# Kernel tuning notes

Measured on AMD Instinct MI355X. Metric: run time of the kernel, lower is better.

## Reference

```python
import jax, jax.numpy as jnp
import numpy as np

B, H, W, D, U = 32, 64, 64, 256, 512


def setup_inputs() -> dict:
    key = jax.random.key(0)
    k1, k2, k3, k4, k5 = jax.random.split(key, 5)
    he_in = np.sqrt(2.0 / D)
    he_u = np.sqrt(2.0 / U)
    return {
        "x": jax.random.normal(k1, (B, H, W, D), dtype=jnp.float32),
        "wax": jax.random.normal(k2, (D, U), dtype=jnp.float32) * he_in,
        "w0": jax.random.normal(k3, (U, U), dtype=jnp.float32) * he_u,
        "w1": jax.random.normal(k4, (U, U), dtype=jnp.float32) * he_u,
        "ba": jax.random.normal(k5, (1, U), dtype=jnp.float32) * 0.01,
    }


def reference(x, wax, w0, w1, ba):
    """2D MDRNN, direction (+1,+1), zero initial state, tanh activation.

    h[i,j] = tanh(x[i,j] @ wax + h[i-1,j] @ w0 + h[i,j-1] @ w1 + ba)
    (out-of-bound neighbors contribute zero, matching the original with
    zero initial state). Returns h at final position (H-1, W-1): (B, U).
    """
    b, h, w, d = x.shape
    u = wax.shape[1]
    # Precompute input contribution for the whole grid: (H, W, B, U)
    zx = jnp.einsum("bhwd,du->hwbu", x, wax) + ba

    def row_step(prev_row, zx_row):
        # prev_row: (W, B, U) = h[i-1, :]; zx_row: (W, B, U)
        pre = zx_row + jnp.einsum("wbu,uv->wbv", prev_row, w0)

        def col_step(h_left, pre_j):
            h_ij = jnp.tanh(pre_j + h_left @ w1)
            return h_ij, h_ij

        _, row = jax.lax.scan(col_step, jnp.zeros((b, u), x.dtype), pre)
        return row, None

    last_row, _ = jax.lax.scan(row_step, jnp.zeros((w, b, u), x.dtype), zx)
    return last_row[-1]  # (B, U)
```

## Files before the change

kernel.cpp:

```cpp
#include <hip/hip_runtime.h>
#include <stdint.h>

#define H_ 64
#define W_ 64
#define D_ 256
#define U_ 512
#define KREC 1024
#define CELL_ELT (32 * U_)

typedef __attribute__((ext_vector_type(8))) _Float16 half8;
typedef __attribute__((ext_vector_type(8))) unsigned short ushort8;
typedef __attribute__((ext_vector_type(4))) float f32x4;

__device__ __forceinline__ unsigned short f2h(float f) {
    _Float16 h = (_Float16)f;
    return __builtin_bit_cast(unsigned short, h);
}

__device__ __forceinline__ int swzo(int r, int o) {
    return o ^ (((r ^ (o >> 7)) & 7) << 4);
}

__global__ void prep_w(const float* __restrict__ w0,
                       const float* __restrict__ w1,
                       unsigned short* __restrict__ wcT2) {
    int n = blockIdx.x;
    for (int k = threadIdx.x; k < KREC; k += blockDim.x) {
        float v = (k < U_) ? w0[(size_t)k * U_ + n] : w1[(size_t)(k - U_) * U_ + n];
        wcT2[(size_t)n * KREC + k] = f2h(v);
    }
}

__global__ void prep_waxT(const float* __restrict__ wax,
                          unsigned short* __restrict__ waxT) {
    int n = blockIdx.x;
    for (int k = threadIdx.x; k < D_; k += blockDim.x)
        waxT[(size_t)n * D_ + k] = f2h(wax[(size_t)k * U_ + n]);
}

__global__ __launch_bounds__(256) void prep_z(
    const float* __restrict__ x,
    const unsigned short* __restrict__ waxT,
    const float* __restrict__ ba,
    unsigned short* __restrict__ zfh)
{
    __shared__ char xs[32 * 512];
    const int cell = blockIdx.x;
    const int t = threadIdx.x, lane = t & 63, wv = t >> 6;
    const int l15 = lane & 15, lh = lane >> 4;
    const int r = t >> 3, c8 = t & 7;

    {
        const float4* src = reinterpret_cast<const float4*>(
            x + (size_t)r * (H_ * W_ * D_) + (size_t)cell * D_ + c8 * 32);
        float4 f[8];
        #pragma unroll
        for (int q = 0; q < 8; ++q) f[q] = src[q];
        #pragma unroll
        for (int s = 0; s < 4; ++s) {
            float4 a = f[2 * s], b = f[2 * s + 1];
            ushort8 o;
            o[0] = f2h(a.x); o[1] = f2h(a.y); o[2] = f2h(a.z); o[3] = f2h(a.w);
            o[4] = f2h(b.x); o[5] = f2h(b.y); o[6] = f2h(b.z); o[7] = f2h(b.w);
            int ob = c8 * 64 + s * 16;
            *reinterpret_cast<ushort8*>(xs + r * 512 + swzo(r, ob)) = o;
        }
    }
    __syncthreads();

    f32x4 zero = {0.f, 0.f, 0.f, 0.f};
    f32x4 acc[2][8];
    #pragma unroll
    for (int m = 0; m < 2; ++m)
        #pragma unroll
        for (int n = 0; n < 8; ++n) acc[m][n] = zero;

    const char* ar0 = xs + l15 * 512;
    const char* ar1 = xs + (16 + l15) * 512;
    #pragma unroll
    for (int ks = 0; ks < 8; ++ks) {
        int ob = ks * 64 + lh * 16;
        int oo = swzo(l15, ob);
        half8 af0 = *reinterpret_cast<const half8*>(ar0 + oo);
        half8 af1 = *reinterpret_cast<const half8*>(ar1 + oo);
        #pragma unroll
        for (int ntg = 0; ntg < 8; ++ntg) {
            int col = wv * 128 + ntg * 16 + l15;
            half8 bf = *reinterpret_cast<const half8*>(waxT + (size_t)col * D_ + ks * 32 + lh * 8);
            acc[0][ntg] = __builtin_amdgcn_mfma_f32_16x16x32_f16(af0, bf, acc[0][ntg], 0, 0, 0);
            acc[1][ntg] = __builtin_amdgcn_mfma_f32_16x16x32_f16(af1, bf, acc[1][ntg], 0, 0, 0);
        }
    }

    #pragma unroll
    for (int s = 0; s < 4; ++s) {
        unsigned short* dst = zfh + (((size_t)cell * 16 + wv * 4 + s) * 64 + lane) * 16;
        float bav0 = ba[wv * 128 + s * 32 + l15];
        float bav1 = ba[wv * 128 + s * 32 + 16 + l15];
        ushort8 oa, ob;
        #pragma unroll
        for (int rr = 0; rr < 4; ++rr) {
            oa[rr]     = f2h(acc[0][s * 2 + 0][rr] + bav0);
            oa[4 + rr] = f2h(acc[0][s * 2 + 1][rr] + bav1);
            ob[rr]     = f2h(acc[1][s * 2 + 0][rr] + bav0);
            ob[4 + rr] = f2h(acc[1][s * 2 + 1][rr] + bav1);
        }
        *reinterpret_cast<ushort8*>(dst)     = oa;
        *reinterpret_cast<ushort8*>(dst + 8) = ob;
    }
}

__global__ __launch_bounds__(256, 1) void mdrnn_persistent(
    const unsigned short* __restrict__ wcT2,
    const unsigned short* __restrict__ zfh,
    unsigned short* __restrict__ hgrid,
    int* flags2,
    float* __restrict__ out)
{
    __shared__ char smb[32 * 2048];
    __shared__ unsigned long long heps64[32 * 32];
    unsigned short* heps16 = reinterpret_cast<unsigned short*>(heps64);

    const int j  = (int)blockIdx.x & 63;
    const int nc = (int)blockIdx.x >> 6;
    const int t = threadIdx.x, lane = t & 63, wv = t >> 6;
    const int l15 = lane & 15, lh = lane >> 4;
    const int r = t >> 3, c8 = t & 7;
    const int gw = nc * 4 + wv;
    const unsigned long long RDY2 = 0x0000000100000001ULL;

    half8 breg[2][32];
    {
        const unsigned short* wb = wcT2 + (size_t)(nc * 128 + wv * 32 + l15) * KREC + lh * 8;
        #pragma unroll
        for (int nt = 0; nt < 2; ++nt)
            #pragma unroll
            for (int ks = 0; ks < 32; ++ks)
                breg[nt][ks] = *reinterpret_cast<const half8*>(wb + (size_t)nt * 16 * KREC + ks * 32);
    }

    #pragma clang loop unroll(disable)
    for (int i = 0; i < H_; ++i) {
        const int cell = i * W_ + j;

        const ushort8* zp = reinterpret_cast<const ushort8*>(
            zfh + (((size_t)cell * 16 + gw) * 64 + lane) * 16);
        ushort8 zv0 = zp[0], zv1 = zp[1];

        if (i > 0 || j > 0) {
            const unsigned long long* fu = reinterpret_cast<const unsigned long long*>(
                flags2 + (size_t)(cell - W_) * 16);
            const unsigned long long* fl = reinterpret_cast<const unsigned long long*>(
                flags2 + (size_t)(cell - 1) * 16);
            const bool nu = (i > 0), nl = (j > 0);
            for (;;) {
                bool ok = true;
                if (nu) {
                    unsigned long long a = __hip_atomic_load(fu,     __ATOMIC_RELAXED, __HIP_MEMORY_SCOPE_AGENT);
                    unsigned long long b = __hip_atomic_load(fu + 1, __ATOMIC_RELAXED, __HIP_MEMORY_SCOPE_AGENT);
                    ok = ok && (a == RDY2) && (b == RDY2);
                }
                if (nl) {
                    unsigned long long a = __hip_atomic_load(fl,     __ATOMIC_RELAXED, __HIP_MEMORY_SCOPE_AGENT);
                    unsigned long long b = __hip_atomic_load(fl + 1, __ATOMIC_RELAXED, __HIP_MEMORY_SCOPE_AGENT);
                    ok = ok && (a == RDY2) && (b == RDY2);
                }
                if (ok) break;
                __builtin_amdgcn_s_sleep(1);
            }
        }
        asm volatile("" ::: "memory");

        if (i > 0) {
            const ushort8* us = reinterpret_cast<const ushort8*>(
                hgrid + (size_t)(cell - W_) * CELL_ELT + (size_t)r * U_ + c8 * 64);
            ushort8 ub[8];
            #pragma unroll
            for (int s = 0; s < 8; ++s) ub[s] = us[s];
            #pragma unroll
            for (int s = 0; s < 8; ++s) {
                int ob = c8 * 128 + s * 16;
                *reinterpret_cast<ushort8*>(smb + r * 2048 + swzo(r, ob)) = ub[s];
            }
        }
        if (j > 0) {
            const ushort8* ls = reinterpret_cast<const ushort8*>(
                hgrid + (size_t)(cell - 1) * CELL_ELT + (size_t)r * U_ + c8 * 64);
            ushort8 lb[8];
            #pragma unroll
            for (int s = 0; s < 8; ++s) lb[s] = ls[s];
            #pragma unroll
            for (int s = 0; s < 8; ++s) {
                int ob = 1024 + c8 * 128 + s * 16;
                *reinterpret_cast<ushort8*>(smb + r * 2048 + swzo(r, ob)) = lb[s];
            }
        }
        __syncthreads();

        f32x4 zero = {0.f, 0.f, 0.f, 0.f};
        f32x4 acc00 = zero, acc01 = zero, acc10 = zero, acc11 = zero;
        const char* ar0 = smb + l15 * 2048;
        const char* ar1 = smb + (16 + l15) * 2048;

#define MSTEP(ks)                                                                                \
        {                                                                                        \
            int ob = (ks) * 64 + lh * 16;                                                        \
            int oo = swzo(l15, ob);                                                              \
            half8 af0 = *reinterpret_cast<const half8*>(ar0 + oo);                               \
            half8 af1 = *reinterpret_cast<const half8*>(ar1 + oo);                               \
            acc00 = __builtin_amdgcn_mfma_f32_16x16x32_f16(af0, breg[0][(ks)], acc00, 0, 0, 0);  \
            acc01 = __builtin_amdgcn_mfma_f32_16x16x32_f16(af0, breg[1][(ks)], acc01, 0, 0, 0);  \
            acc10 = __builtin_amdgcn_mfma_f32_16x16x32_f16(af1, breg[0][(ks)], acc10, 0, 0, 0);  \
            acc11 = __builtin_amdgcn_mfma_f32_16x16x32_f16(af1, breg[1][(ks)], acc11, 0, 0, 0);  \
        }
        if (i > 0) {
            #pragma unroll
            for (int ks = 0; ks < 16; ++ks) MSTEP(ks)
        }
        if (j > 0) {
            #pragma unroll
            for (int ks = 16; ks < 32; ++ks) MSTEP(ks)
        }
#undef MSTEP

        const bool lastcell = (i == H_ - 1) && (j == W_ - 1);
        const int col0 = nc * 128 + wv * 32 + l15;
        const half8 hz0 = __builtin_bit_cast(half8, zv0);
        const half8 hz1 = __builtin_bit_cast(half8, zv1);
        #pragma unroll
        for (int mt = 0; mt < 2; ++mt) {
            f32x4 a0 = mt ? acc10 : acc00;
            f32x4 a1 = mt ? acc11 : acc01;
            half8 hz = mt ? hz1 : hz0;
            #pragma unroll
            for (int rr = 0; rr < 4; ++rr) {
                int row = mt * 16 + lh * 4 + rr;
                float v0 = fminf(fmaxf(a0[rr] + (float)hz[rr],     -15.f), 15.f);
                float v1 = fminf(fmaxf(a1[rr] + (float)hz[4 + rr], -15.f), 15.f);
                float e0 = __expf(2.f * v0), e1 = __expf(2.f * v1);
                float th0 = (e0 - 1.f) / (e0 + 1.f);
                float th1 = (e1 - 1.f) / (e1 + 1.f);
                heps16[row * 128 + wv * 32 + l15]      = f2h(th0);
                heps16[row * 128 + wv * 32 + 16 + l15] = f2h(th1);
                if (lastcell) {
                    out[(size_t)row * U_ + col0]      = th0;
                    out[(size_t)row * U_ + col0 + 16] = th1;
                }
            }
        }
        __syncthreads();

        {
            const int erow = t >> 3, e = t & 7;
            unsigned long long* gq = reinterpret_cast<unsigned long long*>(
                hgrid + (size_t)cell * CELL_ELT + (size_t)erow * U_ + nc * 128);
            #pragma unroll
            for (int q = 0; q < 4; ++q) {
                unsigned long long v = heps64[erow * 32 + q * 8 + e];
                __hip_atomic_store(gq + q * 8 + e, v, __ATOMIC_RELAXED, __HIP_MEMORY_SCOPE_AGENT);
            }
        }

        asm volatile("s_waitcnt vmcnt(0)" ::: "memory");
        __syncthreads();
        if (t == 0)
            __hip_atomic_store(&flags2[(size_t)cell * 16 + nc], 1,
                               __ATOMIC_RELAXED, __HIP_MEMORY_SCOPE_AGENT);
    }
}

extern "C" void kernel_launch(void* const* d_in, const int* in_sizes, int n_in,
                              void* d_out, int out_size, void* d_ws, size_t ws_size,
                              hipStream_t stream) {
    const float* x   = (const float*)d_in[0];
    const float* wax = (const float*)d_in[1];
    const float* w0  = (const float*)d_in[2];
    const float* w1  = (const float*)d_in[3];
    const float* ba  = (const float*)d_in[4];
    float* out = (float*)d_out;

    char* w = (char*)d_ws;
    unsigned short* wcT2   = (unsigned short*)(w);
    unsigned short* waxT   = (unsigned short*)(w + (1u << 20));
    int*            flags2 = (int*)(w + (1u << 20) + (256u << 10));
    unsigned short* zfh    = (unsigned short*)(w + (2u << 20));
    unsigned short* hgrid  = (unsigned short*)(w + (2u << 20) + ((size_t)128 << 20));

    (void)hipMemsetAsync(flags2, 0, (size_t)H_ * W_ * 16 * sizeof(int), stream);
    prep_w   <<<dim3(U_), dim3(256), 0, stream>>>(w0, w1, wcT2);
    prep_waxT<<<dim3(U_), dim3(256), 0, stream>>>(wax, waxT);
    prep_z   <<<dim3(H_ * W_), dim3(256), 0, stream>>>(x, waxT, ba, zfh);
    mdrnn_persistent<<<dim3(W_ * 4), dim3(256), 0, stream>>>(wcT2, zfh, hgrid, flags2, out);
}
```

Before: 996.0 us.

## Group adjacent columns per XCD and poll XCD-local L2 flags for neighbours

```diff
diff --git a/kernel.cpp b/kernel.cpp
--- a/kernel.cpp
+++ b/kernel.cpp
@@ -19,6 +19,18 @@
 
 __device__ __forceinline__ int swzo(int r, int o) {
     return o ^ (((r ^ (o >> 7)) & 7) << 4);
+}
+
+__device__ __forceinline__ int bid_of(int jc, int c) {
+    return (jc >> 3) + ((jc & 7) << 3) + (c << 6);
+}
+
+__device__ __forceinline__ void l2_load2(const unsigned long long* p,
+                                         unsigned long long& a, unsigned long long& b) {
+    asm volatile("global_load_dwordx2 %0, %2, off sc0\n\t"
+                 "global_load_dwordx2 %1, %3, off sc0\n\t"
+                 "s_waitcnt vmcnt(0)"
+                 : "=v"(a), "=v"(b) : "v"(p), "v"(p + 1) : "memory");
 }
 
 __global__ void prep_w(const float* __restrict__ w0,
@@ -79,8 +91,7 @@
     const char* ar1 = xs + (16 + l15) * 512;
     #pragma unroll
     for (int ks = 0; ks < 8; ++ks) {
-        int ob = ks * 64 + lh * 16;
-        int oo = swzo(l15, ob);
+        int oo = swzo(l15, ks * 64 + lh * 16);
         half8 af0 = *reinterpret_cast<const half8*>(ar0 + oo);
         half8 af1 = *reinterpret_cast<const half8*>(ar1 + oo);
         #pragma unroll
@@ -114,21 +125,48 @@
     const unsigned short* __restrict__ wcT2,
     const unsigned short* __restrict__ zfh,
     unsigned short* __restrict__ hgrid,
-    int* flags2,
+    int* flagsLLC, int* flagsL2, int* xcdmap, int* startctr,
     float* __restrict__ out)
 {
     __shared__ char smb[32 * 2048];
     __shared__ unsigned long long heps64[32 * 32];
+    __shared__ int sflag[2];
     unsigned short* heps16 = reinterpret_cast<unsigned short*>(heps64);
 
-    const int j  = (int)blockIdx.x & 63;
-    const int nc = (int)blockIdx.x >> 6;
+    const int blk = (int)blockIdx.x;
+    const int j  = ((blk & 7) << 3) | ((blk >> 3) & 7);
+    const int nc = blk >> 6;
     const int t = threadIdx.x, lane = t & 63, wv = t >> 6;
     const int l15 = lane & 15, lh = lane >> 4;
     const int r = t >> 3, c8 = t & 7;
     const int gw = nc * 4 + wv;
     const unsigned long long RDY2 = 0x0000000100000001ULL;
 
+    __builtin_amdgcn_fence(__ATOMIC_ACQUIRE, "agent");
+    int myxcd;
+    asm volatile("s_getreg_b32 %0, hwreg(HW_REG_XCC_ID)" : "=s"(myxcd));
+    myxcd &= 15;
+    if (t == 0) {
+        __hip_atomic_store(&xcdmap[blk], myxcd + 1, __ATOMIC_RELAXED, __HIP_MEMORY_SCOPE_AGENT);
+        __hip_atomic_fetch_add(startctr, 1, __ATOMIC_RELAXED, __HIP_MEMORY_SCOPE_AGENT);
+        while (__hip_atomic_load(startctr, __ATOMIC_RELAXED, __HIP_MEMORY_SCOPE_AGENT) < 256)
+            __builtin_amdgcn_s_sleep(2);
+        int uf = 1, lf = (j > 0) ? 1 : 0;
+        for (int c = 0; c < 4; ++c) {
+            int v = __hip_atomic_load(&xcdmap[bid_of(j, c)], __ATOMIC_RELAXED, __HIP_MEMORY_SCOPE_AGENT);
+            uf &= (v == myxcd + 1);
+        }
+        if (j > 0)
+            for (int c = 0; c < 4; ++c) {
+                int v = __hip_atomic_load(&xcdmap[bid_of(j - 1, c)], __ATOMIC_RELAXED, __HIP_MEMORY_SCOPE_AGENT);
+                lf &= (v == myxcd + 1);
+            }
+        sflag[0] = uf; sflag[1] = lf;
+    }
+    __syncthreads();
+    const bool uFast = sflag[0] != 0;
+    const bool lFast = sflag[1] != 0;
+
     half8 breg[2][32];
     {
         const unsigned short* wb = wcT2 + (size_t)(nc * 128 + wv * 32 + l15) * KREC + lh * 8;
@@ -148,25 +186,39 @@
         ushort8 zv0 = zp[0], zv1 = zp[1];
 
         if (i > 0 || j > 0) {
-            const unsigned long long* fu = reinterpret_cast<const unsigned long long*>(
-                flags2 + (size_t)(cell - W_) * 16);
-            const unsigned long long* fl = reinterpret_cast<const unsigned long long*>(
-                flags2 + (size_t)(cell - 1) * 16);
             const bool nu = (i > 0), nl = (j > 0);
-            for (;;) {
-                bool ok = true;
-                if (nu) {
-                    unsigned long long a = __hip_atomic_load(fu,     __ATOMIC_RELAXED, __HIP_MEMORY_SCOPE_AGENT);
-                    unsigned long long b = __hip_atomic_load(fu + 1, __ATOMIC_RELAXED, __HIP_MEMORY_SCOPE_AGENT);
-                    ok = ok && (a == RDY2) && (b == RDY2);
+            const unsigned long long* fuF = reinterpret_cast<const unsigned long long*>(
+                flagsL2 + (size_t)(cell - W_) * 16);
+            const unsigned long long* flF = reinterpret_cast<const unsigned long long*>(
+                flagsL2 + (size_t)(cell - 1) * 16);
+            const unsigned long long* fuS = reinterpret_cast<const unsigned long long*>(
+                flagsLLC + (size_t)(cell - W_) * 16);
+            const unsigned long long* flS = reinterpret_cast<const unsigned long long*>(
+                flagsLLC + (size_t)(cell - 1) * 16);
+            bool uok = !nu, lok = !nl;
+            int it = 0;
+            while (!(uok && lok)) {
+                const bool ins = ((it & 63) == 63);
+                if (!uok) {
+                    unsigned long long a, b2;
+                    if (uFast && !ins) l2_load2(fuF, a, b2);
+                    else {
+                        a  = __hip_atomic_load(fuS,     __ATOMIC_RELAXED, __HIP_MEMORY_SCOPE_AGENT);
+                        b2 = __hip_atomic_load(fuS + 1, __ATOMIC_RELAXED, __HIP_MEMORY_SCOPE_AGENT);
+                    }
+                    uok = (a == RDY2) && (b2 == RDY2);
                 }
-                if (nl) {
-                    unsigned long long a = __hip_atomic_load(fl,     __ATOMIC_RELAXED, __HIP_MEMORY_SCOPE_AGENT);
-                    unsigned long long b = __hip_atomic_load(fl + 1, __ATOMIC_RELAXED, __HIP_MEMORY_SCOPE_AGENT);
-                    ok = ok && (a == RDY2) && (b == RDY2);
+                if (!lok) {
+                    unsigned long long a, b2;
+                    if (lFast && !ins) l2_load2(flF, a, b2);
+                    else {
+                        a  = __hip_atomic_load(flS,     __ATOMIC_RELAXED, __HIP_MEMORY_SCOPE_AGENT);
+                        b2 = __hip_atomic_load(flS + 1, __ATOMIC_RELAXED, __HIP_MEMORY_SCOPE_AGENT);
+                    }
+                    lok = (a == RDY2) && (b2 == RDY2);
                 }
-                if (ok) break;
-                __builtin_amdgcn_s_sleep(1);
+                if (!(uok && lok)) __builtin_amdgcn_s_sleep(1);
+                ++it;
             }
         }
         asm volatile("" ::: "memory");
@@ -204,8 +256,7 @@
 
 #define MSTEP(ks)                                                                                \
         {                                                                                        \
-            int ob = (ks) * 64 + lh * 16;                                                        \
-            int oo = swzo(l15, ob);                                                              \
+            int oo = swzo(l15, (ks) * 64 + lh * 16);                                             \
             half8 af0 = *reinterpret_cast<const half8*>(ar0 + oo);                               \
             half8 af1 = *reinterpret_cast<const half8*>(ar1 + oo);                               \
             acc00 = __builtin_amdgcn_mfma_f32_16x16x32_f16(af0, breg[0][(ks)], acc00, 0, 0, 0);  \
@@ -250,21 +301,28 @@
         }
         __syncthreads();
 
-        {
-            const int erow = t >> 3, e = t & 7;
-            unsigned long long* gq = reinterpret_cast<unsigned long long*>(
-                hgrid + (size_t)cell * CELL_ELT + (size_t)erow * U_ + nc * 128);
-            #pragma unroll
-            for (int q = 0; q < 4; ++q) {
-                unsigned long long v = heps64[erow * 32 + q * 8 + e];
-                __hip_atomic_store(gq + q * 8 + e, v, __ATOMIC_RELAXED, __HIP_MEMORY_SCOPE_AGENT);
-            }
-        }
-
+        const int erow = t >> 3, e = t & 7;
+        unsigned long long* gq = reinterpret_cast<unsigned long long*>(
+            hgrid + (size_t)cell * CELL_ELT + (size_t)erow * U_ + nc * 128);
+
+        #pragma unroll
+        for (int q = 0; q < 4; ++q)
+            __hip_atomic_store(gq + q * 8 + e, heps64[erow * 32 + q * 8 + e],
+                               __ATOMIC_RELAXED, __HIP_MEMORY_SCOPE_WORKGROUP);
         asm volatile("s_waitcnt vmcnt(0)" ::: "memory");
         __syncthreads();
         if (t == 0)
-            __hip_atomic_store(&flags2[(size_t)cell * 16 + nc], 1,
+            __hip_atomic_store(&flagsL2[(size_t)cell * 16 + nc], 1,
+                               __ATOMIC_RELAXED, __HIP_MEMORY_SCOPE_WORKGROUP);
+
+        #pragma unroll
+        for (int q = 0; q < 4; ++q)
+            __hip_atomic_store(gq + q * 8 + e, heps64[erow * 32 + q * 8 + e],
+                               __ATOMIC_RELAXED, __HIP_MEMORY_SCOPE_AGENT);
+        asm volatile("s_waitcnt vmcnt(0)" ::: "memory");
+        __syncthreads();
+        if (t == 0)
+            __hip_atomic_store(&flagsLLC[(size_t)cell * 16 + nc], 1,
                                __ATOMIC_RELAXED, __HIP_MEMORY_SCOPE_AGENT);
     }
 }
@@ -280,15 +338,19 @@
     float* out = (float*)d_out;
 
     char* w = (char*)d_ws;
-    unsigned short* wcT2   = (unsigned short*)(w);
-    unsigned short* waxT   = (unsigned short*)(w + (1u << 20));
-    int*            flags2 = (int*)(w + (1u << 20) + (256u << 10));
-    unsigned short* zfh    = (unsigned short*)(w + (2u << 20));
-    unsigned short* hgrid  = (unsigned short*)(w + (2u << 20) + ((size_t)128 << 20));
-
-    (void)hipMemsetAsync(flags2, 0, (size_t)H_ * W_ * 16 * sizeof(int), stream);
+    unsigned short* wcT2     = (unsigned short*)(w);
+    unsigned short* waxT     = (unsigned short*)(w + (1u << 20));
+    int*            flagsLLC = (int*)(w + (1u << 20) + (256u << 10));
+    int*            flagsL2  = (int*)(w + (1u << 20) + (512u << 10));
+    int*            xcdmap   = (int*)(w + (1u << 20) + (768u << 10));
+    int*            startctr = (int*)(w + (1u << 20) + (768u << 10) + 4096);
+    unsigned short* zfh      = (unsigned short*)(w + (2u << 20));
+    unsigned short* hgrid    = (unsigned short*)(w + (2u << 20) + ((size_t)128 << 20));
+
+    (void)hipMemsetAsync(flagsLLC, 0, (768u << 10), stream);
     prep_w   <<<dim3(U_), dim3(256), 0, stream>>>(w0, w1, wcT2);
     prep_waxT<<<dim3(U_), dim3(256), 0, stream>>>(wax, waxT);
     prep_z   <<<dim3(H_ * W_), dim3(256), 0, stream>>>(x, waxT, ba, zfh);
-    mdrnn_persistent<<<dim3(W_ * 4), dim3(256), 0, stream>>>(wcT2, zfh, hgrid, flags2, out);
-}
+    mdrnn_persistent<<<dim3(W_ * 4), dim3(256), 0, stream>>>(
+        wcT2, zfh, hgrid, flagsLLC, flagsL2, xcdmap, startctr, out);
+}
```

Result: slower. 1.884 ms (+89.1%).
